# Kernel optimization log

Hardware: AMD Instinct MI355X
Metric: run time of the kernel (lower is better)

The kernel has to match this reference:

```python
import jax, jax.numpy as jnp
import numpy as np

B, S, D, H = 32, 2048, 256, 256  # batch, seq_len, input_size, hidden_size


def setup_inputs() -> dict:
    key = jax.random.key(0)
    ks = jax.random.split(key, 9)
    s = 0.05  # small init scale to keep gates in a sane range
    return {
        "inputs": jax.random.normal(ks[0], (B, S, D), dtype=jnp.float32),
        "W_ih0": jax.random.normal(ks[1], (3 * H, D), dtype=jnp.float32) * s,
        "W_hh0": jax.random.normal(ks[2], (3 * H, H), dtype=jnp.float32) * s,
        "b_ih0": jax.random.normal(ks[3], (3 * H,), dtype=jnp.float32) * s,
        "b_hh0": jax.random.normal(ks[4], (3 * H,), dtype=jnp.float32) * s,
        "W_ih1": jax.random.normal(ks[5], (3 * H, 2 * H), dtype=jnp.float32) * s,
        "W_hh1": jax.random.normal(ks[6], (3 * H, H), dtype=jnp.float32) * s,
        "b_ih1": jax.random.normal(ks[7], (3 * H,), dtype=jnp.float32) * s,
        "b_hh1": jax.random.normal(ks[8], (3 * H,), dtype=jnp.float32) * s,
    }


def _gru_scan(gx, W_hh, b_hh, reverse):
    """gx: [S,B,3H] precomputed input projections. Returns ([S,B,H] states in
    original time order, [B,H] final carry). lax.scan(reverse=True) stores
    outputs at matching time positions, which matches the module's flip(1)."""
    Hh = W_hh.shape[1]
    h0 = jnp.zeros((gx.shape[1], Hh), gx.dtype)

    def step(h, gx_t):
        gh = h @ W_hh.T + b_hh                      # [B,3H]
        xr, xz, xn = jnp.split(gx_t, 3, axis=-1)
        hr, hz, hn = jnp.split(gh, 3, axis=-1)
        r = jax.nn.sigmoid(xr + hr)
        z = jax.nn.sigmoid(xz + hz)
        n = jnp.tanh(xn + r * hn)
        h_new = (1.0 - z) * n + z * h               # torch.nn.GRUCell update
        return h_new, h_new

    h_last, hs = jax.lax.scan(step, h0, gx, reverse=reverse)
    return hs, h_last


def _bidir_layer(x, W_ih, W_hh, b_ih, b_hh):
    # Precompute all input-to-hidden GEMMs in one batched matmul.
    gx = jnp.einsum('bsd,gd->sbg', x, W_ih) + b_ih  # [S,B,3H]
    # cells_backward is a deepcopy of cells_forward -> identical weights.
    hs_f, hf = _gru_scan(gx, W_hh, b_hh, reverse=False)
    hs_b, hb = _gru_scan(gx, W_hh, b_hh, reverse=True)
    out = jnp.concatenate([hs_f, hs_b], axis=-1).transpose(1, 0, 2)  # [B,S,2H]
    return out, hf, hb


def reference(inputs, W_ih0, W_hh0, b_ih0, b_hh0, W_ih1, W_hh1, b_ih1, b_hh1):
    out0, hf0, hb0 = _bidir_layer(inputs, W_ih0, W_hh0, b_ih0, b_hh0)
    out1, hf1, hb1 = _bidir_layer(out0, W_ih1, W_hh1, b_ih1, b_hh1)
    # h_n order: (layer0 fwd, layer0 bwd, layer1 fwd, layer1 bwd)
    h_n = jnp.stack([hf0, hb0, hf1, hb1])           # [layers*dirs, B, H]
    return out1, h_n
```

## Files before the change

### kernel.cpp

```cpp
#include <hip/hip_runtime.h>

typedef __attribute__((ext_vector_type(4))) float f32x4;
typedef __attribute__((ext_vector_type(8))) short bf16x8;
typedef __attribute__((ext_vector_type(4))) _Float16 f16x4;

constexpr int kB = 32;
constexpr int kS = 2048;
constexpr int kH = 256;
constexpr int kG = 768;

__device__ __forceinline__ short f2bf(float f) {
  unsigned u = __builtin_bit_cast(unsigned, f);
  u += 0x7fffu + ((u >> 16) & 1u);
  return (short)(u >> 16);
}

__device__ __forceinline__ float fast_sigmoid(float x) {
  float e = __builtin_amdgcn_exp2f(x * 1.4426950408889634f);
  return e * __builtin_amdgcn_rcpf(1.0f + e);
}
__device__ __forceinline__ float fast_tanh(float x) {
  float e = __builtin_amdgcn_exp2f(x * 2.8853900817779268f);
  return 1.0f - 2.0f * __builtin_amdgcn_rcpf(1.0f + e);
}

__device__ __forceinline__ void load8(const float* p, float v[8]) {
  const float4 a = *(const float4*)p;
  const float4 b = *(const float4*)(p + 4);
  v[0] = a.x; v[1] = a.y; v[2] = a.z; v[3] = a.w;
  v[4] = b.x; v[5] = b.y; v[6] = b.z; v[7] = b.w;
}

template <int LAYER>
__global__ __launch_bounds__(256) void gemm_gx(
    const void* __restrict__ Av, const float* __restrict__ W,
    const float* __restrict__ b_ih, const float* __restrict__ b_hh,
    _Float16* __restrict__ gx) {
  constexpr int K = (LAYER == 0) ? 256 : 512;
  __shared__ short As[64][40];
  __shared__ short Ws[64][40];
  const int tid = threadIdx.x;
  const int lane = tid & 63, wv = tid >> 6;
  const int quad = lane >> 4, l15 = lane & 15;
  const int m0 = blockIdx.y * 64, n0 = blockIdx.x * 64;
  const int srow = tid >> 2, kq = tid & 3;
  const int am = m0 + srow;
  const int b = am & 31, s = am >> 5;
  const float* Wrow = W + (size_t)(n0 + srow) * K;
  const float* Af = (const float*)Av + ((size_t)b * kS + s) * 256;
  const short* Ab = (const short*)Av + ((size_t)s * 64 + b) * 256;

  f32x4 acc[4] = {};

  for (int k0 = 0; k0 < K; k0 += 32) {
    const int k = k0 + kq * 8;
    short avs[8];
    if constexpr (LAYER == 0) {
      float v[8];
      load8(Af + k, v);
#pragma unroll
      for (int j = 0; j < 8; ++j) avs[j] = f2bf(v[j]);
    } else {
      *(uint4*)avs = *(const uint4*)(Ab + (size_t)(k >> 8) * 8192 + (k & 255));
    }
    float wv8[8];
    load8(Wrow + k, wv8);
    __syncthreads();
#pragma unroll
    for (int j = 0; j < 8; ++j) As[srow][kq * 8 + j] = avs[j];
#pragma unroll
    for (int j = 0; j < 8; ++j) Ws[srow][kq * 8 + j] = f2bf(wv8[j]);
    __syncthreads();
    const bf16x8 bf = *(const bf16x8*)&Ws[wv * 16 + l15][quad * 8];
#pragma unroll
    for (int mt = 0; mt < 4; ++mt) {
      const bf16x8 af = *(const bf16x8*)&As[mt * 16 + l15][quad * 8];
      acc[mt] = __builtin_amdgcn_mfma_f32_16x16x32_bf16(af, bf, acc[mt], 0, 0, 0);
    }
  }
  const int col = n0 + wv * 16 + l15;
  const float bias = b_ih[col] + (col < 512 ? b_hh[col] : 0.0f);
#pragma unroll
  for (int mt = 0; mt < 4; ++mt) {
#pragma unroll
    for (int r = 0; r < 4; ++r) {
      const int m = m0 + mt * 16 + quad * 4 + r;
      gx[((size_t)(m >> 5) * kG + col) * 32 + (m & 31)] = (_Float16)(acc[mt][r] + bias);
    }
  }
}

union Frag8 {
  bf16x8 v;
  uint2 u2[2];
};

template <int LAYER>
__global__ __launch_bounds__(512, 2) void gru_scan(
    const _Float16* __restrict__ gx,
    const float* __restrict__ W_hh,
    const float* __restrict__ b_hh,
    void* __restrict__ outv,
    float* __restrict__ hn) {
  __shared__ short hlds[16][264];
  __shared__ short wlds[768][36];

  const int tid = threadIdx.x;
  const int lane = tid & 63;
  const int w = tid >> 6;
  const int quad = lane >> 4, l15 = lane & 15;
  const int dir = blockIdx.x & 1;
  const int bbase = (blockIdx.x >> 1) * 16;

  for (int i = tid; i < 16 * 264; i += 512) (&hlds[0][0])[i] = 0;

  {
    const int kq = tid & 3, rb = tid >> 2;
#pragma unroll
    for (int j = 0; j < 6; ++j) {
      const int row = rb + j * 128;
      float v[8];
      load8(W_hh + (size_t)row * kH + 224 + kq * 8, v);
#pragma unroll
      for (int e = 0; e < 8; ++e) wlds[row][kq * 8 + e] = f2bf(v[e]);
    }
  }

  const int colH0 = w * 32 + l15;
  bf16x8 Bf[3][2][7];
#pragma unroll
  for (int g3 = 0; g3 < 3; ++g3)
#pragma unroll
    for (int nt = 0; nt < 2; ++nt)
#pragma unroll
      for (int kb = 0; kb < 7; ++kb) {
        const int row = g3 * 256 + colH0 + nt * 16;
        float v[8];
        load8(W_hh + (size_t)row * kH + kb * 32 + quad * 8, v);
        bf16x8 f;
#pragma unroll
        for (int e = 0; e < 8; ++e) f[e] = f2bf(v[e]);
        Bf[g3][nt][kb] = f;
      }

  const float bhn[2] = {b_hh[512 + colH0], b_hh[512 + colH0 + 16]};
  float hprev[8] = {0, 0, 0, 0, 0, 0, 0, 0};

  short* out0 = (short*)outv;
  float* out1 = (float*)outv;

  __syncthreads();

  for (int i = 0; i < kS; ++i) {
    const int t = dir ? (kS - 1 - i) : i;
    const _Float16* gxt = gx + (size_t)t * (kG * 32);

    f16x4 gxv[3][2];
#pragma unroll
    for (int g3 = 0; g3 < 3; ++g3)
#pragma unroll
      for (int nt = 0; nt < 2; ++nt)
        gxv[g3][nt] = *(const f16x4*)(gxt + (size_t)(g3 * 256 + colH0 + nt * 16) * 32 +
                                      bbase + quad * 4);

    f32x4 C0[2] = {}, C1[2] = {}, C2[2] = {};

#define CHAIN(G3, CC)                                                              \
  {                                                                                \
    _Pragma("unroll") for (int kb = 0; kb < 7; ++kb) {                             \
      const bf16x8 af = *(const bf16x8*)&hlds[l15][kb * 32 + quad * 8];            \
      _Pragma("unroll") for (int nt = 0; nt < 2; ++nt) CC[nt] =                    \
          __builtin_amdgcn_mfma_f32_16x16x32_bf16(af, Bf[G3][nt][kb], CC[nt], 0, 0, 0); \
    }                                                                              \
    const bf16x8 af7 = *(const bf16x8*)&hlds[l15][224 + quad * 8];                 \
    _Pragma("unroll") for (int nt = 0; nt < 2; ++nt) {                             \
      Frag8 bf;                                                                    \
      const int row = G3 * 256 + colH0 + nt * 16;                                  \
      bf.u2[0] = *(const uint2*)&wlds[row][quad * 8];                              \
      bf.u2[1] = *(const uint2*)&wlds[row][quad * 8 + 4];                          \
      CC[nt] = __builtin_amdgcn_mfma_f32_16x16x32_bf16(af7, bf.v, CC[nt], 0, 0, 0); \
    }                                                                              \
  }

    CHAIN(0, C0)
    CHAIN(2, C2)

    float rr[2][4];
#pragma unroll
    for (int nt = 0; nt < 2; ++nt)
#pragma unroll
      for (int r = 0; r < 4; ++r)
        rr[nt][r] = fast_sigmoid((float)gxv[0][nt][r] + C0[nt][r]);

    CHAIN(1, C1)

    float nn[2][4];
#pragma unroll
    for (int nt = 0; nt < 2; ++nt)
#pragma unroll
      for (int r = 0; r < 4; ++r)
        nn[nt][r] = fast_tanh((float)gxv[2][nt][r] + rr[nt][r] * (C2[nt][r] + bhn[nt]));

    __syncthreads();

#pragma unroll
    for (int nt = 0; nt < 2; ++nt) {
#pragma unroll
      for (int r = 0; r < 4; ++r) {
        const float zz = fast_sigmoid((float)gxv[1][nt][r] + C1[nt][r]);
        const int e = nt * 4 + r;
        const float h = nn[nt][r] + zz * (hprev[e] - nn[nt][r]);
        hprev[e] = h;
        hlds[quad * 4 + r][colH0 + nt * 16] = f2bf(h);
        if constexpr (LAYER == 1) {
          out1[((size_t)(bbase + quad * 4 + r) * kS + t) * 512 + dir * 256 + colH0 +
               nt * 16] = h;
        }
      }
    }
    __syncthreads();

    if constexpr (LAYER == 0) {
      const int srow = tid >> 5, schunk = tid & 31;
      *(uint4*)(out0 + (((size_t)t * 2 + dir) * 32 + bbase + srow) * 256 + schunk * 8) =
          *(const uint4*)&hlds[srow][schunk * 8];
    }
  }
#undef CHAIN

#pragma unroll
  for (int nt = 0; nt < 2; ++nt)
#pragma unroll
    for (int r = 0; r < 4; ++r)
      hn[(size_t)(dir * kB + bbase + quad * 4 + r) * kH + colH0 + nt * 16] =
          hprev[nt * 4 + r];
}

extern "C" void kernel_launch(void* const* d_in, const int* in_sizes, int n_in,
                              void* d_out, int out_size, void* d_ws, size_t ws_size,
                              hipStream_t stream) {
  const float* x     = (const float*)d_in[0];
  const float* W_ih0 = (const float*)d_in[1];
  const float* W_hh0 = (const float*)d_in[2];
  const float* b_ih0 = (const float*)d_in[3];
  const float* b_hh0 = (const float*)d_in[4];
  const float* W_ih1 = (const float*)d_in[5];
  const float* W_hh1 = (const float*)d_in[6];
  const float* b_ih1 = (const float*)d_in[7];
  const float* b_hh1 = (const float*)d_in[8];

  float* out1 = (float*)d_out;
  float* hn = out1 + (size_t)kB * kS * 512;

  _Float16* gxb = (_Float16*)d_ws;
  short* out0 = (short*)((char*)d_ws + (size_t)kS * kB * kG * 2);

  dim3 ggrid(kG / 64, (kS * kB) / 64);

  gemm_gx<0><<<ggrid, 256, 0, stream>>>(x, W_ih0, b_ih0, b_hh0, gxb);
  gru_scan<0><<<dim3(4), 512, 0, stream>>>(gxb, W_hh0, b_hh0, out0, hn);
  gemm_gx<1><<<ggrid, 256, 0, stream>>>(out0, W_ih1, b_ih1, b_hh1, gxb);
  gru_scan<1><<<dim3(4), 512, 0, stream>>>(gxb, W_hh1, b_hh1, out1, hn + 2 * kB * kH);
}
```

Baseline: 7.832 ms.

## Double-buffer hidden state in LDS and keep more of the n-gate weights in registers

The hidden-state LDS buffer becomes ping-pong double-buffered, which removes one of the two __syncthreads per timestep. The n-gate recurrent weights now stay fully in registers (8 k-blocks), which shrinks the LDS weight tile to the r and z gates. The three gate MFMA chains are interleaved within one k loop, and pointer arithmetic is strength-reduced with incremental pointers. The aim is to cut barrier and LDS latency on the serial recurrence, at the cost of higher register pressure under launch_bounds(512,2).

```diff
diff --git a/kernel.cpp b/kernel.cpp
--- a/kernel.cpp
+++ b/kernel.cpp
@@ -102,8 +102,8 @@
     const float* __restrict__ b_hh,
     void* __restrict__ outv,
     float* __restrict__ hn) {
-  __shared__ short hlds[16][264];
-  __shared__ short wlds[768][36];
+  __shared__ short hlds[2][16][264];
+  __shared__ short wlds[512][36];
 
   const int tid = threadIdx.x;
   const int lane = tid & 63;
@@ -112,12 +112,12 @@
   const int dir = blockIdx.x & 1;
   const int bbase = (blockIdx.x >> 1) * 16;
 
-  for (int i = tid; i < 16 * 264; i += 512) (&hlds[0][0])[i] = 0;
+  for (int i = tid; i < 16 * 264; i += 512) (&hlds[0][0][0])[i] = 0;
 
   {
     const int kq = tid & 3, rb = tid >> 2;
 #pragma unroll
-    for (int j = 0; j < 6; ++j) {
+    for (int j = 0; j < 4; ++j) {
       const int row = rb + j * 128;
       float v[8];
       load8(W_hh + (size_t)row * kH + 224 + kq * 8, v);
@@ -127,21 +127,36 @@
   }
 
   const int colH0 = w * 32 + l15;
-  bf16x8 Bf[3][2][7];
-#pragma unroll
-  for (int g3 = 0; g3 < 3; ++g3)
-#pragma unroll
-    for (int nt = 0; nt < 2; ++nt)
-#pragma unroll
-      for (int kb = 0; kb < 7; ++kb) {
-        const int row = g3 * 256 + colH0 + nt * 16;
-        float v[8];
-        load8(W_hh + (size_t)row * kH + kb * 32 + quad * 8, v);
-        bf16x8 f;
-#pragma unroll
-        for (int e = 0; e < 8; ++e) f[e] = f2bf(v[e]);
-        Bf[g3][nt][kb] = f;
-      }
+
+  bf16x8 Bfr[2][7], Bfz[2][7], Bfn[2][8];
+#pragma unroll
+  for (int nt = 0; nt < 2; ++nt) {
+    const int rowr = 0 * 256 + colH0 + nt * 16;
+    const int rowz = 1 * 256 + colH0 + nt * 16;
+    const int rown = 2 * 256 + colH0 + nt * 16;
+#pragma unroll
+    for (int kb = 0; kb < 7; ++kb) {
+      float v[8];
+      bf16x8 f;
+      load8(W_hh + (size_t)rowr * kH + kb * 32 + quad * 8, v);
+#pragma unroll
+      for (int e = 0; e < 8; ++e) f[e] = f2bf(v[e]);
+      Bfr[nt][kb] = f;
+      load8(W_hh + (size_t)rowz * kH + kb * 32 + quad * 8, v);
+#pragma unroll
+      for (int e = 0; e < 8; ++e) f[e] = f2bf(v[e]);
+      Bfz[nt][kb] = f;
+    }
+#pragma unroll
+    for (int kb = 0; kb < 8; ++kb) {
+      float v[8];
+      bf16x8 f;
+      load8(W_hh + (size_t)rown * kH + kb * 32 + quad * 8, v);
+#pragma unroll
+      for (int e = 0; e < 8; ++e) f[e] = f2bf(v[e]);
+      Bfn[nt][kb] = f;
+    }
+  }
 
   const float bhn[2] = {b_hh[512 + colH0], b_hh[512 + colH0 + 16]};
   float hprev[8] = {0, 0, 0, 0, 0, 0, 0, 0};
@@ -149,84 +164,97 @@
   short* out0 = (short*)outv;
   float* out1 = (float*)outv;
 
+  const ptrdiff_t tstep = dir ? -1 : 1;
+  const int t0 = dir ? (kS - 1) : 0;
+  const _Float16* gp = gx + (size_t)t0 * (kG * 32) + bbase + quad * 4;
+  const ptrdiff_t gstep = tstep * (ptrdiff_t)(kG * 32);
+  int goff[3][2];
+#pragma unroll
+  for (int g3 = 0; g3 < 3; ++g3)
+#pragma unroll
+    for (int nt = 0; nt < 2; ++nt) goff[g3][nt] = (g3 * 256 + colH0 + nt * 16) * 32;
+
+  float* op1 = out1 + ((size_t)(bbase + quad * 4) * kS + t0) * 512 + dir * 256 + colH0;
+  const ptrdiff_t o1step = tstep * 512;
+  const int srow = tid >> 5, schunk = tid & 31;
+  short* op0 = out0 + ((size_t)(t0 * 2 + dir) * 32 + bbase + srow) * 256 + schunk * 8;
+  const ptrdiff_t o0step = tstep * (2 * 32 * 256);
+
   __syncthreads();
 
   for (int i = 0; i < kS; ++i) {
-    const int t = dir ? (kS - 1 - i) : i;
-    const _Float16* gxt = gx + (size_t)t * (kG * 32);
+    const int p = i & 1;
 
     f16x4 gxv[3][2];
 #pragma unroll
     for (int g3 = 0; g3 < 3; ++g3)
 #pragma unroll
       for (int nt = 0; nt < 2; ++nt)
-        gxv[g3][nt] = *(const f16x4*)(gxt + (size_t)(g3 * 256 + colH0 + nt * 16) * 32 +
-                                      bbase + quad * 4);
-
-    f32x4 C0[2] = {}, C1[2] = {}, C2[2] = {};
-
-#define CHAIN(G3, CC)                                                              \
-  {                                                                                \
-    _Pragma("unroll") for (int kb = 0; kb < 7; ++kb) {                             \
-      const bf16x8 af = *(const bf16x8*)&hlds[l15][kb * 32 + quad * 8];            \
-      _Pragma("unroll") for (int nt = 0; nt < 2; ++nt) CC[nt] =                    \
-          __builtin_amdgcn_mfma_f32_16x16x32_bf16(af, Bf[G3][nt][kb], CC[nt], 0, 0, 0); \
-    }                                                                              \
-    const bf16x8 af7 = *(const bf16x8*)&hlds[l15][224 + quad * 8];                 \
-    _Pragma("unroll") for (int nt = 0; nt < 2; ++nt) {                             \
-      Frag8 bf;                                                                    \
-      const int row = G3 * 256 + colH0 + nt * 16;                                  \
-      bf.u2[0] = *(const uint2*)&wlds[row][quad * 8];                              \
-      bf.u2[1] = *(const uint2*)&wlds[row][quad * 8 + 4];                          \
-      CC[nt] = __builtin_amdgcn_mfma_f32_16x16x32_bf16(af7, bf.v, CC[nt], 0, 0, 0); \
-    }                                                                              \
-  }
-
-    CHAIN(0, C0)
-    CHAIN(2, C2)
-
-    float rr[2][4];
+        gxv[g3][nt] = *(const f16x4*)(gp + goff[g3][nt]);
+    gp += gstep;
+
+    f32x4 C[3][2] = {};
+#pragma unroll
+    for (int kb = 0; kb < 8; ++kb) {
+      const bf16x8 af = *(const bf16x8*)&hlds[p][l15][kb * 32 + quad * 8];
+      if (kb < 7) {
+#pragma unroll
+        for (int nt = 0; nt < 2; ++nt) {
+          C[0][nt] = __builtin_amdgcn_mfma_f32_16x16x32_bf16(af, Bfr[nt][kb], C[0][nt], 0, 0, 0);
+          C[1][nt] = __builtin_amdgcn_mfma_f32_16x16x32_bf16(af, Bfz[nt][kb], C[1][nt], 0, 0, 0);
+          C[2][nt] = __builtin_amdgcn_mfma_f32_16x16x32_bf16(af, Bfn[nt][kb], C[2][nt], 0, 0, 0);
+        }
+      } else {
+#pragma unroll
+        for (int nt = 0; nt < 2; ++nt) {
+          C[2][nt] = __builtin_amdgcn_mfma_f32_16x16x32_bf16(af, Bfn[nt][7], C[2][nt], 0, 0, 0);
+          Frag8 bfr, bfz;
+          const int rowr = colH0 + nt * 16;
+          bfr.u2[0] = *(const uint2*)&wlds[rowr][quad * 8];
+          bfr.u2[1] = *(const uint2*)&wlds[rowr][quad * 8 + 4];
+          C[0][nt] = __builtin_amdgcn_mfma_f32_16x16x32_bf16(af, bfr.v, C[0][nt], 0, 0, 0);
+          bfz.u2[0] = *(const uint2*)&wlds[256 + rowr][quad * 8];
+          bfz.u2[1] = *(const uint2*)&wlds[256 + rowr][quad * 8 + 4];
+          C[1][nt] = __builtin_amdgcn_mfma_f32_16x16x32_bf16(af, bfz.v, C[1][nt], 0, 0, 0);
+        }
+      }
+    }
+
+    float rr[2][4], nn[2][4];
 #pragma unroll
     for (int nt = 0; nt < 2; ++nt)
 #pragma unroll
       for (int r = 0; r < 4; ++r)
-        rr[nt][r] = fast_sigmoid((float)gxv[0][nt][r] + C0[nt][r]);
-
-    CHAIN(1, C1)
-
-    float nn[2][4];
+        rr[nt][r] = fast_sigmoid((float)gxv[0][nt][r] + C[0][nt][r]);
 #pragma unroll
     for (int nt = 0; nt < 2; ++nt)
 #pragma unroll
       for (int r = 0; r < 4; ++r)
-        nn[nt][r] = fast_tanh((float)gxv[2][nt][r] + rr[nt][r] * (C2[nt][r] + bhn[nt]));
-
-    __syncthreads();
+        nn[nt][r] = fast_tanh((float)gxv[2][nt][r] + rr[nt][r] * (C[2][nt][r] + bhn[nt]));
 
 #pragma unroll
     for (int nt = 0; nt < 2; ++nt) {
 #pragma unroll
       for (int r = 0; r < 4; ++r) {
-        const float zz = fast_sigmoid((float)gxv[1][nt][r] + C1[nt][r]);
+        const float zz = fast_sigmoid((float)gxv[1][nt][r] + C[1][nt][r]);
         const int e = nt * 4 + r;
         const float h = nn[nt][r] + zz * (hprev[e] - nn[nt][r]);
         hprev[e] = h;
-        hlds[quad * 4 + r][colH0 + nt * 16] = f2bf(h);
+        hlds[1 - p][quad * 4 + r][colH0 + nt * 16] = f2bf(h);
         if constexpr (LAYER == 1) {
-          out1[((size_t)(bbase + quad * 4 + r) * kS + t) * 512 + dir * 256 + colH0 +
-               nt * 16] = h;
+          op1[(size_t)r * (kS * 512) + nt * 16] = h;
         }
       }
     }
+    if constexpr (LAYER == 1) op1 += o1step;
+
     __syncthreads();
 
     if constexpr (LAYER == 0) {
-      const int srow = tid >> 5, schunk = tid & 31;
-      *(uint4*)(out0 + (((size_t)t * 2 + dir) * 32 + bbase + srow) * 256 + schunk * 8) =
-          *(const uint4*)&hlds[srow][schunk * 8];
-    }
-  }
-#undef CHAIN
+      *(uint4*)op0 = *(const uint4*)&hlds[1 - p][srow][schunk * 8];
+      op0 += o0step;
+    }
+  }
 
 #pragma unroll
   for (int nt = 0; nt < 2; ++nt)
```

After: 7.933 ms. Within noise of the previous version (+1.3%).
